# Optimization experiments

Measured on AMD Instinct MI355X. Metric: run time of the kernel, lower is better.

## Reference

```python
import math
import jax, jax.numpy as jnp
import numpy as np

S = 2048
D_MOD = 1024
D_K = 64
D_V = 64
H = 16
MASKED = True


def setup_inputs() -> dict:
    key = jax.random.key(0)
    ks = jax.random.split(key, 11)
    sc_in = 1.0 / math.sqrt(D_MOD)
    sc_o = 1.0 / math.sqrt(H * D_V)
    return {
        "Q_input": jax.random.normal(ks[0], (S, D_MOD), jnp.float32),
        "K_input": jax.random.normal(ks[1], (S, D_MOD), jnp.float32),
        "V_input": jax.random.normal(ks[2], (S, D_MOD), jnp.float32),
        # stacked per-head Linear params (torch Linear: y = x @ W.T + b)
        "WQw": jax.random.uniform(ks[3], (H, D_K, D_MOD), jnp.float32, -sc_in, sc_in),
        "WQb": jax.random.uniform(ks[4], (H, D_K), jnp.float32, -sc_in, sc_in),
        "WKw": jax.random.uniform(ks[5], (H, D_K, D_MOD), jnp.float32, -sc_in, sc_in),
        "WKb": jax.random.uniform(ks[6], (H, D_K), jnp.float32, -sc_in, sc_in),
        "WVw": jax.random.uniform(ks[7], (H, D_V, D_MOD), jnp.float32, -sc_in, sc_in),
        "WVb": jax.random.uniform(ks[8], (H, D_V), jnp.float32, -sc_in, sc_in),
        "WOw": jax.random.uniform(ks[9], (D_MOD, H * D_V), jnp.float32, -sc_o, sc_o),
        "WOb": jax.random.uniform(ks[10], (D_MOD,), jnp.float32, -sc_o, sc_o),
    }


def reference(Q_input, K_input, V_input, WQw, WQb, WKw, WKb, WVw, WVb, WOw, WOb):
    # per-head projections, batched over heads: [H, S, d]
    q = jnp.einsum("sd,hkd->hsk", Q_input, WQw) + WQb[:, None, :]
    k = jnp.einsum("sd,hkd->hsk", K_input, WKw) + WKb[:, None, :]
    v = jnp.einsum("sd,hvd->hsv", V_input, WVw) + WVb[:, None, :]
    # raw scores [H, S, T]
    qk = jnp.einsum("hsk,htk->hst", q, k)
    if MASKED:
        qk = jnp.tril(qk)  # torch.tril: zero (not -inf) upper triangle
    # torch log_softmax(dim=0) on each [S, T] matrix -> axis 1 of [H, S, T]
    scores = jax.nn.log_softmax(qk / math.sqrt(D_K), axis=1)
    attn = jnp.einsum("hst,htv->hsv", scores, v)  # [H, S, d_v]
    # torch.cat(head_attns, dim=1) -> [S, H*d_v], head-major feature order
    Z = jnp.transpose(attn, (1, 0, 2)).reshape(S, H * D_V)
    return Z @ WOw.T + WOb
```

## Files before the change

### kernel.cpp

```cpp
#include <hip/hip_runtime.h>
#include <math.h>
#include <stdint.h>

#define S 2048
#define DMOD 1024
#define H 16

typedef unsigned short ushort_t;
typedef short bf16x8 __attribute__((ext_vector_type(8)));
typedef float f32x4 __attribute__((ext_vector_type(4)));

#define SW(r) ((((r) & 7)) ^ ((((r) >> 3) & 3) << 1))

__device__ __forceinline__ ushort_t f2b(float f) {
    union { float f; unsigned u; } x; x.f = f;
    return (ushort_t)((x.u + 0x7FFFu + ((x.u >> 16) & 1u)) >> 16);
}
__device__ __forceinline__ ushort_t f2b_fast(float f) {
    union { float f; unsigned u; } x; x.f = f;
    return (ushort_t)((x.u + 0x8000u) >> 16);
}
__device__ __forceinline__ float b2f(ushort_t b) {
    union { unsigned u; float f; } x; x.u = ((unsigned)b) << 16;
    return x.f;
}
__device__ __forceinline__ void gld16(const ushort_t* g, ushort_t* l) {
    __builtin_amdgcn_global_load_lds(
        (const __attribute__((address_space(1))) unsigned int*)g,
        (__attribute__((address_space(3))) unsigned int*)l, 16, 0, 0);
}

__global__ __launch_bounds__(256) void prep_all(
    const float* q, const float* k, const float* v,
    const float* wq, const float* wk, const float* wv, const float* wo,
    ushort_t* qo, ushort_t* ko, ushort_t* vo,
    ushort_t* wqo, ushort_t* wko, ushort_t* wvo, ushort_t* woo,
    float* __restrict__ attn_raw, float* __restrict__ out,
    float* __restrict__ sumexp, float* __restrict__ corr)
{
    const int seg = blockIdx.y;
    const int bx = blockIdx.x;
    if (seg >= 10) {
        const float4 z4 = {0.f, 0.f, 0.f, 0.f};
        if (seg < 12) {
            *(float4*)(attn_raw + (((size_t)(seg - 10) * 1024 + bx) * 256 + threadIdx.x) * 4) = z4;
        } else if (seg < 14) {
            *(float4*)(out + (((size_t)(seg - 12) * 1024 + bx) * 256 + threadIdx.x) * 4) = z4;
        } else if (bx < 32) {
            int e = (bx * 256 + threadIdx.x) * 4;
            float4 vv = {(float)(e & 2047), (float)((e + 1) & 2047),
                         (float)((e + 2) & 2047), (float)((e + 3) & 2047)};
            *(float4*)(sumexp + e) = vv;
        } else if (bx == 32) {
            *(float4*)(corr + threadIdx.x * 4) = z4;
        }
        return;
    }
    const float* src; ushort_t* dst; size_t off = 0;
    const size_t M1 = (size_t)1 << 20;
    if (seg < 2)       { src = q;  dst = qo;  off = (size_t)seg * M1; }
    else if (seg < 4)  { src = k;  dst = ko;  off = (size_t)(seg - 2) * M1; }
    else if (seg < 6)  { src = v;  dst = vo;  off = (size_t)(seg - 4) * M1; }
    else if (seg == 6) { src = wq; dst = wqo; }
    else if (seg == 7) { src = wk; dst = wko; }
    else if (seg == 8) { src = wv; dst = wvo; }
    else               { src = wo; dst = woo; }
    size_t i = off + ((size_t)bx * 256 + threadIdx.x) * 4;
    float4 f = *(const float4*)(src + i);
    union { uint2 u2; ushort_t us[4]; } o;
    o.us[0] = f2b(f.x); o.us[1] = f2b(f.y); o.us[2] = f2b(f.z); o.us[3] = f2b(f.w);
    *(uint2*)(dst + i) = o.u2;
}

__global__ __launch_bounds__(256) void gemm_qkv(
    const ushort_t* __restrict__ A0, const ushort_t* __restrict__ A1,
    const ushort_t* __restrict__ A2, const ushort_t* __restrict__ Wqkv,
    const float* __restrict__ b0, const float* __restrict__ b1,
    const float* __restrict__ b2,
    ushort_t* __restrict__ qbb, ushort_t* __restrict__ kbb,
    ushort_t* __restrict__ vt)
{
    __shared__ ushort_t As[128 * 64];
    __shared__ ushort_t Bs[64 * 64];
    const int tid = threadIdx.x;
    const int lane = tid & 63, wid = tid >> 6;
    const int quad = lane >> 4, l15 = lane & 15;
    const int wr = wid >> 1, wc = wid & 1;
    const int m0 = blockIdx.y * 128;
    const int n0 = blockIdx.x * 64;
    const int seg = n0 >> 10;
    const int nloc = n0 & 1023;
    const ushort_t* A = seg == 0 ? A0 : (seg == 1 ? A1 : A2);
    const float* bias = seg == 0 ? b0 : (seg == 1 ? b1 : b2);

    const f32x4 fz = {0.f, 0.f, 0.f, 0.f};
    f32x4 acc[4][2];
#pragma unroll
    for (int i = 0; i < 4; ++i) { acc[i][0] = fz; acc[i][1] = fz; }

    for (int k0 = 0; k0 < DMOD; k0 += 64) {
        __syncthreads();
#pragma unroll
        for (int i = 0; i < 4; ++i) {
            int c = i * 256 + tid, row = c >> 3, kcl = c & 7;
            gld16(A + (size_t)(m0 + row) * DMOD + k0 + (kcl ^ SW(row)) * 8, &As[c * 8]);
        }
#pragma unroll
        for (int i = 0; i < 2; ++i) {
            int c = i * 256 + tid, row = c >> 3, kcl = c & 7;
            gld16(Wqkv + (size_t)(n0 + row) * DMOD + k0 + (kcl ^ SW(row)) * 8, &Bs[c * 8]);
        }
        __syncthreads();
#pragma unroll
        for (int kc = 0; kc < 2; ++kc) {
            bf16x8 af[4], bfr[2];
#pragma unroll
            for (int mi = 0; mi < 4; ++mi) {
                int row = wr * 64 + mi * 16 + l15;
                af[mi] = *(const bf16x8*)&As[row * 64 + ((kc * 4 + quad) ^ SW(row)) * 8];
            }
#pragma unroll
            for (int ni = 0; ni < 2; ++ni) {
                int row = wc * 32 + ni * 16 + l15;
                bfr[ni] = *(const bf16x8*)&Bs[row * 64 + ((kc * 4 + quad) ^ SW(row)) * 8];
            }
#pragma unroll
            for (int mi = 0; mi < 4; ++mi)
#pragma unroll
                for (int ni = 0; ni < 2; ++ni)
                    acc[mi][ni] = __builtin_amdgcn_mfma_f32_16x16x32_bf16(
                        af[mi], bfr[ni], acc[mi][ni], 0, 0, 0);
        }
    }

    if (seg < 2) {
        ushort_t* C = seg == 0 ? qbb : kbb;
#pragma unroll
        for (int mi = 0; mi < 4; ++mi)
#pragma unroll
            for (int ni = 0; ni < 2; ++ni) {
                int gn = nloc + wc * 32 + ni * 16 + l15;
                float bv = bias[gn];
#pragma unroll
                for (int r = 0; r < 4; ++r) {
                    int gm = m0 + wr * 64 + mi * 16 + quad * 4 + r;
                    C[(size_t)gm * DMOD + gn] = f2b(acc[mi][ni][r] + bv);
                }
            }
    } else {
#pragma unroll
        for (int mi = 0; mi < 4; ++mi)
#pragma unroll
            for (int ni = 0; ni < 2; ++ni) {
                int gn = nloc + wc * 32 + ni * 16 + l15;
                float bv = bias[gn];
                int gmb = m0 + wr * 64 + mi * 16 + quad * 4;
                union { uint2 u2; ushort_t us[4]; } o;
#pragma unroll
                for (int r = 0; r < 4; ++r) o.us[r] = f2b(acc[mi][ni][r] + bv);
                *(uint2*)&vt[(size_t)gn * S + gmb] = o.u2;
            }
    }
}

__global__ __launch_bounds__(512, 4) void attn_mfma(
    const ushort_t* __restrict__ qb, const ushort_t* __restrict__ kb,
    const ushort_t* __restrict__ vt, float* __restrict__ attn_raw,
    float* __restrict__ sumexp)
{
    __shared__ ushort_t QPs[128 * 64];
    __shared__ ushort_t Ks[2][4096];
    __shared__ ushort_t Vs[2][4096];
    __shared__ float    sacc[1024];

    const int slot = blockIdx.x;
    const int h = slot >> 4, u = slot & 15;
    const int rnd = blockIdx.y;
    int si, tbeg, tend;
    if (rnd == 0) { si = 15 - u; tbeg = 0; tend = si + 1; }
    else {
        si = u;
        const int b0 = u + 1, Bc = (u + 2) >> 1;
        if (rnd == 1) { tbeg = b0; tend = b0 + Bc; }
        else          { tbeg = b0 + Bc; tend = 2 * u + 2; }
    }
    if (tbeg >= tend) return;
    const int s0 = si * 128;

    const int tid = threadIdx.x;
    const int lane = tid & 63, w = tid >> 6;
    const int quad = lane >> 4, l15 = lane & 15;
    const int sband = s0 + w * 16;
    const int nv = (tend - tbeg) * 64;

    const ushort_t* qh = qb + h * 64;
    const ushort_t* kh = kb + h * 64;
    const ushort_t* vh = vt + (size_t)(h * 64) * S;

#pragma unroll
    for (int i = 0; i < 2; ++i) {
        int c = i * 512 + tid, row = c >> 3, kcl = c & 7;
        gld16(qh + (size_t)(s0 + row) * DMOD + (kcl ^ SW(row)) * 8, &QPs[c * 8]);
    }
    {
        int t0 = tbeg * 64;
        int row = tid >> 3, kcl = tid & 7;
        gld16(kh + (size_t)(t0 + row) * DMOD + (kcl ^ SW(row)) * 8, &Ks[0][tid * 8]);
        gld16(vh + (size_t)row * S + t0 + (kcl ^ SW(row)) * 8, &Vs[0][tid * 8]);
    }
    for (int i = tid; i < nv; i += 512) sacc[i] = 0.f;
    __syncthreads();

    bf16x8 aq[2];
    {
        int rq = w * 16 + l15;
#pragma unroll
        for (int kc = 0; kc < 2; ++kc)
            aq[kc] = *(const bf16x8*)&QPs[rq * 64 + ((kc * 4 + quad) ^ SW(rq)) * 8];
    }

    const f32x4 fz = {0.f, 0.f, 0.f, 0.f};
    f32x4 oacc[4];
#pragma unroll
    for (int ni = 0; ni < 4; ++ni) oacc[ni] = fz;
    bool any_live = false;

    for (int it = tbeg; it < tend; ++it) {
        const int p = (it - tbeg) & 1;
        const int t0 = it * 64;
        if (it + 1 < tend) {
            int t1 = t0 + 64;
            int row = tid >> 3, kcl = tid & 7;
            gld16(kh + (size_t)(t1 + row) * DMOD + (kcl ^ SW(row)) * 8, &Ks[1 - p][tid * 8]);
            gld16(vh + (size_t)row * S + t1 + (kcl ^ SW(row)) * 8, &Vs[1 - p][tid * 8]);
        }

        if (t0 < sband + 16) {
            any_live = true;
            f32x4 xf[4];
#pragma unroll
            for (int ti = 0; ti < 4; ++ti) xf[ti] = fz;
#pragma unroll
            for (int kc = 0; kc < 2; ++kc) {
#pragma unroll
                for (int ti = 0; ti < 4; ++ti) {
                    int rk = ti * 16 + l15;
                    bf16x8 bk = *(const bf16x8*)&Ks[p][rk * 64 + ((kc * 4 + quad) ^ SW(rk)) * 8];
                    xf[ti] = __builtin_amdgcn_mfma_f32_16x16x32_bf16(aq[kc], bk, xf[ti], 0, 0, 0);
                }
            }

            const bool clean = (t0 + 63 <= sband);
            const int s_q = sband + quad * 4;
#pragma unroll
            for (int ti = 0; ti < 4; ++ti) {
                int t_g = t0 + ti * 16 + l15;
                float es = 0.f;
                if (clean) {
#pragma unroll
                    for (int r = 0; r < 4; ++r) {
                        float xv = xf[ti][r] * 0.125f;
                        es += __expf(xv);
                        xf[ti][r] = xv;
                    }
                } else {
#pragma unroll
                    for (int r = 0; r < 4; ++r) {
                        float xv = xf[ti][r] * 0.125f;
                        bool live = (s_q + r >= t_g);
                        xv = live ? xv : 0.f;
                        es += live ? __expf(xv) : 0.f;
                        xf[ti][r] = xv;
                    }
                }
                es += __shfl_xor(es, 16, 64);
                es += __shfl_xor(es, 32, 64);
                if (quad == 0) atomicAdd(&sacc[(it - tbeg) * 64 + ti * 16 + l15], es);
#pragma unroll
                for (int r = 0; r < 4; ++r) {
                    int sl = w * 16 + quad * 4 + r;
                    int tc = ti * 16 + l15;
                    QPs[sl * 64 + ((tc >> 3) ^ SW(sl)) * 8 + (tc & 7)] = f2b_fast(xf[ti][r]);
                }
            }

#pragma unroll
            for (int kc = 0; kc < 2; ++kc) {
                int rp = w * 16 + l15;
                bf16x8 ap = *(const bf16x8*)&QPs[rp * 64 + ((kc * 4 + quad) ^ SW(rp)) * 8];
#pragma unroll
                for (int ni = 0; ni < 4; ++ni) {
                    int rv = ni * 16 + l15;
                    bf16x8 bv = *(const bf16x8*)&Vs[p][rv * 64 + ((kc * 4 + quad) ^ SW(rv)) * 8];
                    oacc[ni] = __builtin_amdgcn_mfma_f32_16x16x32_bf16(ap, bv, oacc[ni], 0, 0, 0);
                }
            }
        }
        __syncthreads();
    }

    for (int i = tid; i < nv; i += 512)
        atomicAdd(&sumexp[h * S + tbeg * 64 + i], sacc[i]);
    if (any_live) {
#pragma unroll
        for (int ni = 0; ni < 4; ++ni)
#pragma unroll
            for (int r = 0; r < 4; ++r) {
                int s_g = s0 + w * 16 + quad * 4 + r;
                atomicAdd(&attn_raw[(size_t)s_g * DMOD + h * 64 + ni * 16 + l15],
                          oacc[ni][r]);
            }
    }
}

__global__ __launch_bounds__(256) void corr_kernel(
    const float* __restrict__ sumexp, const ushort_t* __restrict__ vt,
    float* __restrict__ corr)
{
    __shared__ float ls[S];
    const int h = blockIdx.x >> 2;
    const int r0 = blockIdx.x * 16;
    const int tid = threadIdx.x;
    for (int t = tid; t < S; t += 256)
        ls[t] = __logf(sumexp[h * S + t]);
    __syncthreads();
    const int w = tid >> 6, lane = tid & 63;
#pragma unroll
    for (int rr = 0; rr < 4; ++rr) {
        int r = r0 + w * 4 + rr;
        float acc = 0.f;
#pragma unroll
        for (int i = 0; i < 4; ++i) {
            int t = i * 512 + lane * 8;
            bf16x8 vv = *(const bf16x8*)&vt[(size_t)r * S + t];
#pragma unroll
            for (int j = 0; j < 8; ++j)
                acc += ls[t + j] * b2f((ushort_t)vv[j]);
        }
#pragma unroll
        for (int d = 1; d < 64; d <<= 1) acc += __shfl_xor(acc, d, 64);
        if (lane == 0) corr[r] = acc;
    }
}

__global__ __launch_bounds__(256) void convert_Z(
    const float* __restrict__ attn_raw, const float* __restrict__ corr,
    ushort_t* __restrict__ Zb)
{
    size_t i = ((size_t)blockIdx.x * 256 + threadIdx.x) * 4;
    float4 f = *(const float4*)(attn_raw + i);
    int c = (int)(i & (DMOD - 1));
    union { uint2 u2; ushort_t us[4]; } o;
    o.us[0] = f2b(f.x - corr[c]);
    o.us[1] = f2b(f.y - corr[c + 1]);
    o.us[2] = f2b(f.z - corr[c + 2]);
    o.us[3] = f2b(f.w - corr[c + 3]);
    *(uint2*)(Zb + i) = o.u2;
}

__global__ __launch_bounds__(256) void gemm_out(
    const ushort_t* __restrict__ A, const ushort_t* __restrict__ W,
    const float* __restrict__ bias, float* __restrict__ C)
{
    __shared__ ushort_t As[128 * 64];
    __shared__ ushort_t Bs[64 * 64];
    const int tid = threadIdx.x;
    const int lane = tid & 63, wid = tid >> 6;
    const int quad = lane >> 4, l15 = lane & 15;
    const int wr = wid >> 1, wc = wid & 1;
    const int m0 = blockIdx.y * 128, n0 = blockIdx.x * 64;
    const int kbeg = blockIdx.z * 512, kend = kbeg + 512;

    const f32x4 fz = {0.f, 0.f, 0.f, 0.f};
    f32x4 acc[4][2];
#pragma unroll
    for (int i = 0; i < 4; ++i) { acc[i][0] = fz; acc[i][1] = fz; }

    for (int k0 = kbeg; k0 < kend; k0 += 64) {
        __syncthreads();
#pragma unroll
        for (int i = 0; i < 4; ++i) {
            int c = i * 256 + tid, row = c >> 3, kcl = c & 7;
            gld16(A + (size_t)(m0 + row) * DMOD + k0 + (kcl ^ SW(row)) * 8, &As[c * 8]);
        }
#pragma unroll
        for (int i = 0; i < 2; ++i) {
            int c = i * 256 + tid, row = c >> 3, kcl = c & 7;
            gld16(W + (size_t)(n0 + row) * DMOD + k0 + (kcl ^ SW(row)) * 8, &Bs[c * 8]);
        }
        __syncthreads();
#pragma unroll
        for (int kc = 0; kc < 2; ++kc) {
            bf16x8 af[4], bfr[2];
#pragma unroll
            for (int mi = 0; mi < 4; ++mi) {
                int row = wr * 64 + mi * 16 + l15;
                af[mi] = *(const bf16x8*)&As[row * 64 + ((kc * 4 + quad) ^ SW(row)) * 8];
            }
#pragma unroll
            for (int ni = 0; ni < 2; ++ni) {
                int row = wc * 32 + ni * 16 + l15;
                bfr[ni] = *(const bf16x8*)&Bs[row * 64 + ((kc * 4 + quad) ^ SW(row)) * 8];
            }
#pragma unroll
            for (int mi = 0; mi < 4; ++mi)
#pragma unroll
                for (int ni = 0; ni < 2; ++ni)
                    acc[mi][ni] = __builtin_amdgcn_mfma_f32_16x16x32_bf16(
                        af[mi], bfr[ni], acc[mi][ni], 0, 0, 0);
        }
    }
#pragma unroll
    for (int mi = 0; mi < 4; ++mi)
#pragma unroll
        for (int ni = 0; ni < 2; ++ni) {
            int gn = n0 + wc * 32 + ni * 16 + l15;
            float bv = (kbeg == 0) ? bias[gn] : 0.f;
#pragma unroll
            for (int r = 0; r < 4; ++r) {
                int gm = m0 + wr * 64 + mi * 16 + quad * 4 + r;
                atomicAdd(&C[(size_t)gm * DMOD + gn], acc[mi][ni][r] + bv);
            }
        }
}

extern "C" void kernel_launch(void* const* d_in, const int* in_sizes, int n_in,
                              void* d_out, int out_size, void* d_ws, size_t ws_size,
                              hipStream_t stream) {
    const float* Qin = (const float*)d_in[0];
    const float* Kin = (const float*)d_in[1];
    const float* Vin = (const float*)d_in[2];
    const float* WQw = (const float*)d_in[3];
    const float* WQb = (const float*)d_in[4];
    const float* WKw = (const float*)d_in[5];
    const float* WKb = (const float*)d_in[6];
    const float* WVw = (const float*)d_in[7];
    const float* WVb = (const float*)d_in[8];
    const float* WOw = (const float*)d_in[9];
    const float* WOb = (const float*)d_in[10];

    float* ws = (float*)d_ws;
    const size_t M1 = (size_t)1 << 20;
    ushort_t* qbb  = (ushort_t*)(ws);
    ushort_t* kbb  = (ushort_t*)(ws + M1);
    ushort_t* vt   = (ushort_t*)(ws + 2 * M1);
    ushort_t* wqkv = (ushort_t*)(ws + 3 * M1);
    ushort_t* wob  = (ushort_t*)(ws + 4 * M1 + M1 / 2);
    ushort_t* Qbin = (ushort_t*)(ws + 5 * M1);
    ushort_t* Kbin = (ushort_t*)(ws + 6 * M1);
    ushort_t* Vbin = (ushort_t*)(ws + 7 * M1);
    float* sumexp   = ws + 8 * M1;
    float* corr     = ws + 8 * M1 + H * S;
    float* attn_raw = ws + 9 * M1;
    ushort_t* Zb    = (ushort_t*)(ws + 5 * M1);

    prep_all<<<dim3(1024, 15), 256, 0, stream>>>(
        Qin, Kin, Vin, WQw, WKw, WVw, WOw,
        Qbin, Kbin, Vbin,
        wqkv, wqkv + (size_t)1024 * 1024, wqkv + (size_t)2 * 1024 * 1024, wob,
        attn_raw, (float*)d_out, sumexp, corr);

    gemm_qkv<<<dim3(48, 16), 256, 0, stream>>>(
        Qbin, Kbin, Vbin, wqkv, WQb, WKb, WVb, qbb, kbb, vt);

    attn_mfma<<<dim3(256, 3), 512, 0, stream>>>(qbb, kbb, vt, attn_raw, sumexp);

    corr_kernel<<<64, 256, 0, stream>>>(sumexp, vt, corr);
    convert_Z<<<2048, 256, 0, stream>>>(attn_raw, corr, Zb);

    gemm_out<<<dim3(16, 16, 2), 256, 0, stream>>>(Zb, wob, WOb, (float*)d_out);
}
```

Before: 188.9 us.

## Switch attention tile loop to 32x32x16 MFMA with band/half-T wave split

Reorganises the causal attention kernel so each wave owns a 32-row query band and one 32-column half of each key tile. The QK^T and PV products move from 16x16x32 to 32x32x16 bf16 MFMA instructions, with matching fragment indexing, masking and P write-back into LDS. The aim is fewer MFMA issues and fewer LDS fragment loads per tile. In exchange, the two waves of a band now both atomically add partial outputs to the same rows, which doubles global atomics on attn_raw. Causal masking is also applied at a coarser 32-column granularity per wave.

```diff
diff --git a/kernel.cpp b/kernel.cpp
--- a/kernel.cpp
+++ b/kernel.cpp
@@ -9,6 +9,7 @@
 typedef unsigned short ushort_t;
 typedef short bf16x8 __attribute__((ext_vector_type(8)));
 typedef float f32x4 __attribute__((ext_vector_type(4)));
+typedef float f32x16 __attribute__((ext_vector_type(16)));
 
 #define SW(r) ((((r) & 7)) ^ ((((r) >> 3) & 3) << 1))
 
@@ -189,8 +190,10 @@
 
     const int tid = threadIdx.x;
     const int lane = tid & 63, w = tid >> 6;
-    const int quad = lane >> 4, l15 = lane & 15;
-    const int sband = s0 + w * 16;
+    const int band = w >> 1, th = w & 1;
+    const int l31 = lane & 31, hi1 = lane >> 5, hi4 = hi1 * 4;
+    const int bandb = band * 32;
+    const int sb = s0 + bandb;
     const int nv = (tend - tbeg) * 64;
 
     const ushort_t* qh = qb + h * 64;
@@ -211,23 +214,25 @@
     for (int i = tid; i < nv; i += 512) sacc[i] = 0.f;
     __syncthreads();
 
-    bf16x8 aq[2];
+    bf16x8 aq[4];
     {
-        int rq = w * 16 + l15;
-#pragma unroll
-        for (int kc = 0; kc < 2; ++kc)
-            aq[kc] = *(const bf16x8*)&QPs[rq * 64 + ((kc * 4 + quad) ^ SW(rq)) * 8];
-    }
-
-    const f32x4 fz = {0.f, 0.f, 0.f, 0.f};
-    f32x4 oacc[4];
-#pragma unroll
-    for (int ni = 0; ni < 4; ++ni) oacc[ni] = fz;
+        int rq = bandb + l31;
+#pragma unroll
+        for (int kc = 0; kc < 4; ++kc)
+            aq[kc] = *(const bf16x8*)&QPs[rq * 64 + (((kc * 2 + hi1)) ^ SW(rq)) * 8];
+    }
+    __syncthreads();
+
+    const f32x16 fz16 = {0.f,0.f,0.f,0.f,0.f,0.f,0.f,0.f,
+                         0.f,0.f,0.f,0.f,0.f,0.f,0.f,0.f};
+    f32x16 oacc[2];
+    oacc[0] = fz16; oacc[1] = fz16;
     bool any_live = false;
 
     for (int it = tbeg; it < tend; ++it) {
         const int p = (it - tbeg) & 1;
         const int t0 = it * 64;
+        const int t0w = t0 + th * 32;
         if (it + 1 < tend) {
             int t1 = t0 + 64;
             int row = tid >> 3, kcl = tid & 7;
@@ -235,64 +240,60 @@
             gld16(vh + (size_t)row * S + t1 + (kcl ^ SW(row)) * 8, &Vs[1 - p][tid * 8]);
         }
 
-        if (t0 < sband + 16) {
+        if (t0w < sb + 32) {
             any_live = true;
-            f32x4 xf[4];
-#pragma unroll
-            for (int ti = 0; ti < 4; ++ti) xf[ti] = fz;
-#pragma unroll
-            for (int kc = 0; kc < 2; ++kc) {
-#pragma unroll
-                for (int ti = 0; ti < 4; ++ti) {
-                    int rk = ti * 16 + l15;
-                    bf16x8 bk = *(const bf16x8*)&Ks[p][rk * 64 + ((kc * 4 + quad) ^ SW(rk)) * 8];
-                    xf[ti] = __builtin_amdgcn_mfma_f32_16x16x32_bf16(aq[kc], bk, xf[ti], 0, 0, 0);
+            f32x16 xf = fz16;
+#pragma unroll
+            for (int kc = 0; kc < 4; ++kc) {
+                int rk = th * 32 + l31;
+                bf16x8 bk = *(const bf16x8*)&Ks[p][rk * 64 + (((kc * 2 + hi1)) ^ SW(rk)) * 8];
+                xf = __builtin_amdgcn_mfma_f32_32x32x16_bf16(aq[kc], bk, xf, 0, 0, 0);
+            }
+
+            const bool clean = (t0w + 31 <= sb);
+            const int t_g = t0w + l31;
+            float es = 0.f;
+            if (clean) {
+#pragma unroll
+                for (int j = 0; j < 16; ++j) {
+                    float xv = xf[j] * 0.125f;
+                    es += __expf(xv);
+                    xf[j] = xv;
                 }
-            }
-
-            const bool clean = (t0 + 63 <= sband);
-            const int s_q = sband + quad * 4;
-#pragma unroll
-            for (int ti = 0; ti < 4; ++ti) {
-                int t_g = t0 + ti * 16 + l15;
-                float es = 0.f;
-                if (clean) {
-#pragma unroll
-                    for (int r = 0; r < 4; ++r) {
-                        float xv = xf[ti][r] * 0.125f;
-                        es += __expf(xv);
-                        xf[ti][r] = xv;
-                    }
-                } else {
-#pragma unroll
-                    for (int r = 0; r < 4; ++r) {
-                        float xv = xf[ti][r] * 0.125f;
-                        bool live = (s_q + r >= t_g);
-                        xv = live ? xv : 0.f;
-                        es += live ? __expf(xv) : 0.f;
-                        xf[ti][r] = xv;
-                    }
+            } else {
+#pragma unroll
+                for (int j = 0; j < 16; ++j) {
+                    float xv = xf[j] * 0.125f;
+                    int s_g = sb + (j & 3) + 8 * (j >> 2) + hi4;
+                    bool live = (s_g >= t_g);
+                    xv = live ? xv : 0.f;
+                    es += live ? __expf(xv) : 0.f;
+                    xf[j] = xv;
                 }
-                es += __shfl_xor(es, 16, 64);
-                es += __shfl_xor(es, 32, 64);
-                if (quad == 0) atomicAdd(&sacc[(it - tbeg) * 64 + ti * 16 + l15], es);
-#pragma unroll
-                for (int r = 0; r < 4; ++r) {
-                    int sl = w * 16 + quad * 4 + r;
-                    int tc = ti * 16 + l15;
-                    QPs[sl * 64 + ((tc >> 3) ^ SW(sl)) * 8 + (tc & 7)] = f2b_fast(xf[ti][r]);
+            }
+            es += __shfl_xor(es, 32, 64);
+            if (lane < 32) atomicAdd(&sacc[(it - tbeg) * 64 + th * 32 + l31], es);
+
+            {
+                int chp = (th * 4 + (l31 >> 3));
+                int bytep = (lane & 7);
+#pragma unroll
+                for (int j = 0; j < 16; ++j) {
+                    int sl = bandb + (j & 3) + 8 * (j >> 2) + hi4;
+                    QPs[sl * 64 + (chp ^ SW(sl)) * 8 + bytep] = f2b_fast(xf[j]);
                 }
             }
 
 #pragma unroll
-            for (int kc = 0; kc < 2; ++kc) {
-                int rp = w * 16 + l15;
-                bf16x8 ap = *(const bf16x8*)&QPs[rp * 64 + ((kc * 4 + quad) ^ SW(rp)) * 8];
-#pragma unroll
-                for (int ni = 0; ni < 4; ++ni) {
-                    int rv = ni * 16 + l15;
-                    bf16x8 bv = *(const bf16x8*)&Vs[p][rv * 64 + ((kc * 4 + quad) ^ SW(rv)) * 8];
-                    oacc[ni] = __builtin_amdgcn_mfma_f32_16x16x32_bf16(ap, bv, oacc[ni], 0, 0, 0);
+            for (int kc2 = 0; kc2 < 2; ++kc2) {
+                int rp = bandb + l31;
+                int ch = th * 4 + kc2 * 2 + hi1;
+                bf16x8 ap = *(const bf16x8*)&QPs[rp * 64 + ((ch ^ SW(rp))) * 8];
+#pragma unroll
+                for (int vti = 0; vti < 2; ++vti) {
+                    int rv = vti * 32 + l31;
+                    bf16x8 bv = *(const bf16x8*)&Vs[p][rv * 64 + ((ch ^ SW(rv))) * 8];
+                    oacc[vti] = __builtin_amdgcn_mfma_f32_32x32x16_bf16(ap, bv, oacc[vti], 0, 0, 0);
                 }
             }
         }
@@ -303,12 +304,12 @@
         atomicAdd(&sumexp[h * S + tbeg * 64 + i], sacc[i]);
     if (any_live) {
 #pragma unroll
-        for (int ni = 0; ni < 4; ++ni)
-#pragma unroll
-            for (int r = 0; r < 4; ++r) {
-                int s_g = s0 + w * 16 + quad * 4 + r;
-                atomicAdd(&attn_raw[(size_t)s_g * DMOD + h * 64 + ni * 16 + l15],
-                          oacc[ni][r]);
+        for (int vti = 0; vti < 2; ++vti)
+#pragma unroll
+            for (int j = 0; j < 16; ++j) {
+                int s_g = sb + (j & 3) + 8 * (j >> 2) + hi4;
+                atomicAdd(&attn_raw[(size_t)s_g * DMOD + h * 64 + vti * 32 + l31],
+                          oacc[vti][j]);
             }
     }
 }
```

After: 195.7 us. +3.6%, slower.

## Enlarge attention query tile to 256 rows and rebalance causal work split

Applied to the files above, without the earlier changes.

The attention kernel now gives each block 256 query rows instead of 128, with each wave covering two 16-row tiles. Every K/V fragment loaded from shared memory therefore feeds two MFMAs, halving K/V traffic per unit of compute. The causal work is redistributed into 512 blocks: each head/row-tile pair is split into four equal key chunks, and the row-tile order is mirrored across the two halves of the heads to balance load. The trade-offs are higher register and LDS use per block, which lowers occupancy, and more masked waste inside the larger diagonal tiles.

```diff
diff --git a/kernel.cpp b/kernel.cpp
--- a/kernel.cpp
+++ b/kernel.cpp
@@ -168,39 +168,33 @@
     const ushort_t* __restrict__ vt, float* __restrict__ attn_raw,
     float* __restrict__ sumexp)
 {
-    __shared__ ushort_t QPs[128 * 64];
+    __shared__ ushort_t QPs[256 * 64];
     __shared__ ushort_t Ks[2][4096];
     __shared__ ushort_t Vs[2][4096];
-    __shared__ float    sacc[1024];
-
-    const int slot = blockIdx.x;
-    const int h = slot >> 4, u = slot & 15;
-    const int rnd = blockIdx.y;
-    int si, tbeg, tend;
-    if (rnd == 0) { si = 15 - u; tbeg = 0; tend = si + 1; }
-    else {
-        si = u;
-        const int b0 = u + 1, Bc = (u + 2) >> 1;
-        if (rnd == 1) { tbeg = b0; tend = b0 + Bc; }
-        else          { tbeg = b0 + Bc; tend = 2 * u + 2; }
-    }
-    if (tbeg >= tend) return;
-    const int s0 = si * 128;
+    __shared__ float    sacc[512];
+
+    const int bx = blockIdx.x;
+    const int slot = bx >> 2, c = bx & 3;
+    const int h = slot >> 3, iidx = slot & 7;
+    const int si = (h < 8) ? iidx : 7 - iidx;
+    const int csz = si + 1;
+    const int tbeg = c * csz, tend = tbeg + csz;
+    const int s0 = si * 256;
 
     const int tid = threadIdx.x;
     const int lane = tid & 63, w = tid >> 6;
     const int quad = lane >> 4, l15 = lane & 15;
-    const int sband = s0 + w * 16;
-    const int nv = (tend - tbeg) * 64;
+    const int sband = s0 + w * 32;
+    const int nv = csz * 64;
 
     const ushort_t* qh = qb + h * 64;
     const ushort_t* kh = kb + h * 64;
     const ushort_t* vh = vt + (size_t)(h * 64) * S;
 
 #pragma unroll
-    for (int i = 0; i < 2; ++i) {
-        int c = i * 512 + tid, row = c >> 3, kcl = c & 7;
-        gld16(qh + (size_t)(s0 + row) * DMOD + (kcl ^ SW(row)) * 8, &QPs[c * 8]);
+    for (int i = 0; i < 4; ++i) {
+        int cc = i * 512 + tid, row = cc >> 3, kcl = cc & 7;
+        gld16(qh + (size_t)(s0 + row) * DMOD + (kcl ^ SW(row)) * 8, &QPs[cc * 8]);
     }
     {
         int t0 = tbeg * 64;
@@ -211,18 +205,21 @@
     for (int i = tid; i < nv; i += 512) sacc[i] = 0.f;
     __syncthreads();
 
-    bf16x8 aq[2];
-    {
-        int rq = w * 16 + l15;
+    bf16x8 aq[2][2];
+#pragma unroll
+    for (int rt = 0; rt < 2; ++rt) {
+        int rq = w * 32 + rt * 16 + l15;
 #pragma unroll
         for (int kc = 0; kc < 2; ++kc)
-            aq[kc] = *(const bf16x8*)&QPs[rq * 64 + ((kc * 4 + quad) ^ SW(rq)) * 8];
+            aq[rt][kc] = *(const bf16x8*)&QPs[rq * 64 + ((kc * 4 + quad) ^ SW(rq)) * 8];
     }
 
     const f32x4 fz = {0.f, 0.f, 0.f, 0.f};
-    f32x4 oacc[4];
-#pragma unroll
-    for (int ni = 0; ni < 4; ++ni) oacc[ni] = fz;
+    f32x4 oacc[2][4];
+#pragma unroll
+    for (int rt = 0; rt < 2; ++rt)
+#pragma unroll
+        for (int ni = 0; ni < 4; ++ni) oacc[rt][ni] = fz;
     bool any_live = false;
 
     for (int it = tbeg; it < tend; ++it) {
@@ -235,64 +232,80 @@
             gld16(vh + (size_t)row * S + t1 + (kcl ^ SW(row)) * 8, &Vs[1 - p][tid * 8]);
         }
 
-        if (t0 < sband + 16) {
+        if (t0 < sband + 32) {
             any_live = true;
-            f32x4 xf[4];
-#pragma unroll
-            for (int ti = 0; ti < 4; ++ti) xf[ti] = fz;
+            f32x4 xf[2][4];
+#pragma unroll
+            for (int rt = 0; rt < 2; ++rt)
+#pragma unroll
+                for (int ti = 0; ti < 4; ++ti) xf[rt][ti] = fz;
 #pragma unroll
             for (int kc = 0; kc < 2; ++kc) {
 #pragma unroll
                 for (int ti = 0; ti < 4; ++ti) {
                     int rk = ti * 16 + l15;
                     bf16x8 bk = *(const bf16x8*)&Ks[p][rk * 64 + ((kc * 4 + quad) ^ SW(rk)) * 8];
-                    xf[ti] = __builtin_amdgcn_mfma_f32_16x16x32_bf16(aq[kc], bk, xf[ti], 0, 0, 0);
-                }
-            }
-
-            const bool clean = (t0 + 63 <= sband);
-            const int s_q = sband + quad * 4;
-#pragma unroll
-            for (int ti = 0; ti < 4; ++ti) {
-                int t_g = t0 + ti * 16 + l15;
-                float es = 0.f;
-                if (clean) {
+#pragma unroll
+                    for (int rt = 0; rt < 2; ++rt)
+                        xf[rt][ti] = __builtin_amdgcn_mfma_f32_16x16x32_bf16(
+                            aq[rt][kc], bk, xf[rt][ti], 0, 0, 0);
+                }
+            }
+
+#pragma unroll
+            for (int rt = 0; rt < 2; ++rt) {
+                const int sb_rt = sband + rt * 16;
+                const bool clean = (t0 + 63 <= sb_rt);
+                const int s_q = sb_rt + quad * 4;
+#pragma unroll
+                for (int ti = 0; ti < 4; ++ti) {
+                    int t_g = t0 + ti * 16 + l15;
+                    float es = 0.f;
+                    if (clean) {
+#pragma unroll
+                        for (int r = 0; r < 4; ++r) {
+                            float xv = xf[rt][ti][r] * 0.125f;
+                            es += __expf(xv);
+                            xf[rt][ti][r] = xv;
+                        }
+                    } else {
+#pragma unroll
+                        for (int r = 0; r < 4; ++r) {
+                            float xv = xf[rt][ti][r] * 0.125f;
+                            bool live = (s_q + r >= t_g);
+                            xv = live ? xv : 0.f;
+                            es += live ? __expf(xv) : 0.f;
+                            xf[rt][ti][r] = xv;
+                        }
+                    }
+                    es += __shfl_xor(es, 16, 64);
+                    es += __shfl_xor(es, 32, 64);
+                    if (quad == 0) atomicAdd(&sacc[(it - tbeg) * 64 + ti * 16 + l15], es);
 #pragma unroll
                     for (int r = 0; r < 4; ++r) {
-                        float xv = xf[ti][r] * 0.125f;
-                        es += __expf(xv);
-                        xf[ti][r] = xv;
+                        int sl = w * 32 + rt * 16 + quad * 4 + r;
+                        int tc = ti * 16 + l15;
+                        QPs[sl * 64 + ((tc >> 3) ^ SW(sl)) * 8 + (tc & 7)] = f2b_fast(xf[rt][ti][r]);
                     }
-                } else {
-#pragma unroll
-                    for (int r = 0; r < 4; ++r) {
-                        float xv = xf[ti][r] * 0.125f;
-                        bool live = (s_q + r >= t_g);
-                        xv = live ? xv : 0.f;
-                        es += live ? __expf(xv) : 0.f;
-                        xf[ti][r] = xv;
-                    }
-                }
-                es += __shfl_xor(es, 16, 64);
-                es += __shfl_xor(es, 32, 64);
-                if (quad == 0) atomicAdd(&sacc[(it - tbeg) * 64 + ti * 16 + l15], es);
-#pragma unroll
-                for (int r = 0; r < 4; ++r) {
-                    int sl = w * 16 + quad * 4 + r;
-                    int tc = ti * 16 + l15;
-                    QPs[sl * 64 + ((tc >> 3) ^ SW(sl)) * 8 + (tc & 7)] = f2b_fast(xf[ti][r]);
                 }
             }
 
 #pragma unroll
             for (int kc = 0; kc < 2; ++kc) {
-                int rp = w * 16 + l15;
-                bf16x8 ap = *(const bf16x8*)&QPs[rp * 64 + ((kc * 4 + quad) ^ SW(rp)) * 8];
+                bf16x8 ap[2];
+#pragma unroll
+                for (int rt = 0; rt < 2; ++rt) {
+                    int rp = w * 32 + rt * 16 + l15;
+                    ap[rt] = *(const bf16x8*)&QPs[rp * 64 + ((kc * 4 + quad) ^ SW(rp)) * 8];
+                }
 #pragma unroll
                 for (int ni = 0; ni < 4; ++ni) {
                     int rv = ni * 16 + l15;
                     bf16x8 bv = *(const bf16x8*)&Vs[p][rv * 64 + ((kc * 4 + quad) ^ SW(rv)) * 8];
-                    oacc[ni] = __builtin_amdgcn_mfma_f32_16x16x32_bf16(ap, bv, oacc[ni], 0, 0, 0);
+#pragma unroll
+                    for (int rt = 0; rt < 2; ++rt)
+                        oacc[rt][ni] = __builtin_amdgcn_mfma_f32_16x16x32_bf16(
+                            ap[rt], bv, oacc[rt][ni], 0, 0, 0);
                 }
             }
         }
@@ -303,13 +316,15 @@
         atomicAdd(&sumexp[h * S + tbeg * 64 + i], sacc[i]);
     if (any_live) {
 #pragma unroll
-        for (int ni = 0; ni < 4; ++ni)
-#pragma unroll
-            for (int r = 0; r < 4; ++r) {
-                int s_g = s0 + w * 16 + quad * 4 + r;
-                atomicAdd(&attn_raw[(size_t)s_g * DMOD + h * 64 + ni * 16 + l15],
-                          oacc[ni][r]);
-            }
+        for (int rt = 0; rt < 2; ++rt)
+#pragma unroll
+            for (int ni = 0; ni < 4; ++ni)
+#pragma unroll
+                for (int r = 0; r < 4; ++r) {
+                    int s_g = s0 + w * 32 + rt * 16 + quad * 4 + r;
+                    atomicAdd(&attn_raw[(size_t)s_g * DMOD + h * 64 + ni * 16 + l15],
+                              oacc[rt][ni][r]);
+                }
     }
 }
 
@@ -463,7 +478,7 @@
     gemm_qkv<<<dim3(48, 16), 256, 0, stream>>>(
         Qbin, Kbin, Vbin, wqkv, WQb, WKb, WVb, qbb, kbb, vt);
 
-    attn_mfma<<<dim3(256, 3), 512, 0, stream>>>(qbb, kbb, vt, attn_raw, sumexp);
+    attn_mfma<<<512, 512, 0, stream>>>(qbb, kbb, vt, attn_raw, sumexp);
 
     corr_kernel<<<64, 256, 0, stream>>>(sumexp, vt, corr);
     convert_Z<<<2048, 256, 0, stream>>>(attn_raw, corr, Zb);
```

After: 227.7 us. 20.5% more time.
